# Kernel tuning notes

Measured on AMD Instinct MI355X. Metric: run time of the kernel, lower is better.

Reference implementation:

```python
import jax, jax.numpy as jnp
import numpy as np

N, E, G = 200000, 600000, 1024
NF_IN, EF_IN, H = 32, 16, 512
BN_EPS = 1e-5


def _bn(x, gamma, beta):
    # eval-mode BatchNorm1d with running_mean=0, running_var=1
    return x * (gamma / jnp.sqrt(1.0 + BN_EPS)) + beta


def setup_inputs() -> dict:
    key = jax.random.key(0)
    ks = jax.random.split(key, 32)
    s = 0.05
    inp = {
        'nf': jax.random.normal(ks[0], (N, NF_IN), jnp.float32),
        'ef': jax.random.normal(ks[1], (E, EF_IN), jnp.float32),
        'gf': jax.random.normal(ks[2], (G, H), jnp.float32),
        'device_params': jax.random.uniform(ks[3], (N,), jnp.float32),
        'node_y': jax.random.randint(ks[4], (N,), 0, 9),
        'batch_idx': jnp.sort(jax.random.randint(ks[5], (N,), 0, G)),
        'edge_index': jax.random.randint(ks[6], (2, E), 0, N),
        'nf_w1': jax.random.normal(ks[7], (NF_IN + 9, H), jnp.float32) * s,
        'nf_b1': jax.random.normal(ks[8], (H,), jnp.float32) * s,
        'nf_g1': jax.random.uniform(ks[9], (H,), jnp.float32, 0.5, 1.5),
        'nf_be1': jax.random.normal(ks[10], (H,), jnp.float32) * s,
        'nf_w2': jax.random.normal(ks[11], (H, H), jnp.float32) * s,
        'nf_b2': jax.random.normal(ks[12], (H,), jnp.float32) * s,
        'ef_w1': jax.random.normal(ks[13], (EF_IN, H), jnp.float32) * s,
        'ef_b1': jax.random.normal(ks[14], (H,), jnp.float32) * s,
        'ef_g1': jax.random.uniform(ks[15], (H,), jnp.float32, 0.5, 1.5),
        'ef_be1': jax.random.normal(ks[16], (H,), jnp.float32) * s,
        'ef_w2': jax.random.normal(ks[17], (H, H), jnp.float32) * s,
        'ef_b2': jax.random.normal(ks[18], (H,), jnp.float32) * s,
        'ow1': jax.random.normal(ks[19], (H, H), jnp.float32) * s,
        'ob1': jax.random.normal(ks[20], (H,), jnp.float32) * s,
        'og1': jax.random.uniform(ks[21], (H,), jnp.float32, 0.5, 1.5),
        'obe1': jax.random.normal(ks[22], (H,), jnp.float32) * s,
        'ow2': jax.random.normal(ks[23], (H, H), jnp.float32) * s,
        'ob2': jax.random.normal(ks[24], (H,), jnp.float32) * s,
        'og2': jax.random.uniform(ks[25], (H,), jnp.float32, 0.5, 1.5),
        'obe2': jax.random.normal(ks[26], (H,), jnp.float32) * s,
        'ow3': jax.random.normal(ks[27], (H, 2), jnp.float32) * s,
        'ob3': jax.random.normal(ks[28], (2,), jnp.float32) * s,
    }
    return inp


def reference(nf, ef, gf, device_params, node_y, batch_idx, edge_index,
              nf_w1, nf_b1, nf_g1, nf_be1, nf_w2, nf_b2,
              ef_w1, ef_b1, ef_g1, ef_be1, ef_w2, ef_b2,
              ow1, ob1, og1, obe1, ow2, ob2, og2, obe2, ow3, ob3):
    num_graphs = gf.shape[0]
    gelu = lambda x: jax.nn.gelu(x, approximate=False)  # torch nn.GELU default

    # DeviceParam_MLP: augment node features with scaled one-hot of node class
    nf_aug = jnp.concatenate(
        [nf, jax.nn.one_hot(node_y, 9, dtype=nf.dtype) * device_params[:, None]],
        axis=-1)  # [N, nf_in+9]
    h_n = gelu(_bn(nf_aug @ nf_w1 + nf_b1, nf_g1, nf_be1)) @ nf_w2 + nf_b2  # [N,H]
    h_e = gelu(_bn(ef @ ef_w1 + ef_b1, ef_g1, ef_be1)) @ ef_w2 + ef_b2      # [E,H]

    # two scatter_add pools into graph features
    gh = gf
    gh = gh + jax.ops.segment_sum(h_n, batch_idx, num_segments=num_graphs)
    edge_graph = batch_idx[edge_index[0]]  # graph id of each edge's source node
    gh = gh + jax.ops.segment_sum(h_e, edge_graph, num_segments=num_graphs)

    # output MLP (layer_num=3): two hidden blocks + final Linear -> 2
    x = gelu(_bn(gh @ ow1 + ob1, og1, obe1))
    x = gelu(_bn(x @ ow2 + ob2, og2, obe2))
    return x @ ow3 + ob3  # [G, 2]
```

## Files before the change

kernel.cpp:

```cpp
#include <hip/hip_runtime.h>
#include <hip/hip_bf16.h>

#define NN 200000
#define NE 600000
#define NG 1024
#define HH 512
#define ECAP 1024

typedef short short8 __attribute__((ext_vector_type(8)));
typedef float f32x4 __attribute__((ext_vector_type(4)));
typedef float f32x2 __attribute__((ext_vector_type(2)));

__device__ __forceinline__ unsigned short f2bf(float f){
  unsigned u = __float_as_uint(f);
  u += 0x7fffu + ((u >> 16) & 1u);
  return (unsigned short)(u >> 16);
}
__device__ __forceinline__ float bf2f(unsigned short h){
  return __uint_as_float(((unsigned)h) << 16);
}

__device__ __forceinline__ short8 cvt8pk(float4 a, float4 b){
  union { short8 s; __hip_bfloat162 h[4]; } u;
  u.h[0] = __float22bfloat162_rn(make_float2(a.x, a.y));
  u.h[1] = __float22bfloat162_rn(make_float2(a.z, a.w));
  u.h[2] = __float22bfloat162_rn(make_float2(b.x, b.y));
  u.h[3] = __float22bfloat162_rn(make_float2(b.z, b.w));
  return u.s;
}

__device__ __forceinline__ void split8(const float* v, short8* hi, short8* lo){
  union { short8 s; __hip_bfloat162 h[4]; unsigned u[4]; } H, L;
#pragma unroll
  for (int p=0;p<4;++p){
    float a = v[2*p], b = v[2*p+1];
    H.h[p] = __float22bfloat162_rn(make_float2(a, b));
    unsigned hu = H.u[p];
    L.h[p] = __float22bfloat162_rn(make_float2(a - __uint_as_float(hu << 16),
                                               b - __uint_as_float(hu & 0xffff0000u)));
  }
  *hi = H.s; *lo = L.s;
}

__device__ __forceinline__ float gelu_f(float x){
  float p = __builtin_fmaf(x*x, -0.10294325f, -2.3022085f);
  float e = __builtin_amdgcn_exp2f(x * p);
  return x * __builtin_amdgcn_rcpf(1.0f + e);
}

__device__ __forceinline__ float gelu_poly(float x,
    float C0, float C1, float C2, float C3, float C4, float C5, float C6, float C7){
  float u = x*x;
  float s = __builtin_fmaf(u, 0.125f, -1.0f);
  float p = C7;
  p = __builtin_fmaf(p, s, C6); p = __builtin_fmaf(p, s, C5);
  p = __builtin_fmaf(p, s, C4); p = __builtin_fmaf(p, s, C3);
  p = __builtin_fmaf(p, s, C2); p = __builtin_fmaf(p, s, C1);
  p = __builtin_fmaf(p, s, C0);
  return __builtin_fmaf(x, 0.5f, p);
}

__device__ __forceinline__ void gelu2_acc(f32x2 x, f32x2& dst,
    float C0, float C1, float C2, float C3, float C4, float C5, float C6, float C7){
  f32x2 u = x*x;
  f32x2 s = __builtin_elementwise_fma(u, (f32x2)0.125f, (f32x2)(-1.0f));
  f32x2 p = (f32x2)C7;
  p = __builtin_elementwise_fma(p, s, (f32x2)C6);
  p = __builtin_elementwise_fma(p, s, (f32x2)C5);
  p = __builtin_elementwise_fma(p, s, (f32x2)C4);
  p = __builtin_elementwise_fma(p, s, (f32x2)C3);
  p = __builtin_elementwise_fma(p, s, (f32x2)C2);
  p = __builtin_elementwise_fma(p, s, (f32x2)C1);
  p = __builtin_elementwise_fma(p, s, (f32x2)C0);
  dst += __builtin_elementwise_fma(x, (f32x2)0.5f, p);
}

__global__ __launch_bounds__(256) void kpre(
    const float* __restrict__ nfw1, const float* __restrict__ nfb1,
    const float* __restrict__ nfg1, const float* __restrict__ nfbe1,
    const float* __restrict__ efw1, const float* __restrict__ efb1,
    const float* __restrict__ efg1, const float* __restrict__ efbe1,
    unsigned short* __restrict__ w1nT, unsigned short* __restrict__ w1eT,
    float* __restrict__ b1n, float* __restrict__ b1e,
    const int* __restrict__ bidx, int* __restrict__ nstart,
    int* __restrict__ cnt, float* __restrict__ pcoef,
    const float* __restrict__ nf, const float* __restrict__ dp,
    const int* __restrict__ ny,
    unsigned short* __restrict__ nfb, unsigned short* __restrict__ hb){
  const float rs = 0.99999500003750f;
  int b = blockIdx.x, t = threadIdx.x;
  if (b < 196){
    int tid = b*256 + t;
    if (tid < 512*64){
      int c = tid >> 6, k = tid & 63;
      float w = (k < 41) ? nfw1[k*HH + c] * nfg1[c] * rs : 0.0f;
      w1nT[tid] = f2bf(w);
    } else if (tid < 512*96){
      int u = tid - 512*64; int c = u >> 5, k = u & 31;
      float w = (k < 16) ? efw1[k*HH + c] * efg1[c] * rs : 0.0f;
      w1eT[u] = f2bf(w);
    } else if (tid < 512*96 + 512){
      int c = tid - 512*96;
      b1n[c] = nfb1[c]*nfg1[c]*rs + nfbe1[c];
    } else if (tid < 512*96 + 1024){
      int c = tid - (512*96 + 512);
      b1e[c] = efb1[c]*efg1[c]*rs + efbe1[c];
    }
  } else if (b < 978){
    int i = (b-196)*256 + t;
    if (i < NN){
      int g0 = bidx[i];
      int g1 = (i+1 < NN) ? bidx[i+1] : NG;
      for (int g = g0+1; g <= g1; ++g) nstart[g] = i+1;
      if (i == 0) for (int g = 0; g <= g0; ++g) nstart[g] = 0;
    }
  } else if (b == 978){
    cnt[t] = 0; cnt[t+256] = 0; cnt[t+512] = 0; cnt[t+768] = 0;
  } else if (b == 979){
    if (t == 0){
      double th[8], fj[8];
      for (int j=0;j<8;++j){
        th[j] = 3.14159265358979323846*((double)j + 0.5)/8.0;
        double cs = cos(th[j]);
        double u = 8.0*(cs + 1.0);
        double v = sqrt(u);
        fj[j] = 0.5*v*erf(v*0.70710678118654752);
      }
      double c[8];
      for (int k=0;k<8;++k){
        double sm = 0.0;
        for (int j=0;j<8;++j) sm += fj[j]*cos((double)k*th[j]);
        c[k] = 0.25*sm;
      }
      c[0] *= 0.5;
      const double T[8][8] = {
        { 1, 0,  0,  0,   0,    0,  0,  0},
        { 0, 1,  0,  0,   0,    0,  0,  0},
        {-1, 0,  2,  0,   0,    0,  0,  0},
        { 0,-3,  0,  4,   0,    0,  0,  0},
        { 1, 0, -8,  0,   8,    0,  0,  0},
        { 0, 5,  0,-20,   0,   16,  0,  0},
        {-1, 0, 18,  0, -48,    0, 32,  0},
        { 0,-7,  0, 56,   0, -112,  0, 64}};
      double m[8] = {0,0,0,0,0,0,0,0};
      for (int k=0;k<8;++k)
        for (int i=0;i<8;++i) m[i] += c[k]*T[k][i];
      double p0 = m[0]-m[1]+m[2]-m[3]+m[4]-m[5]+m[6]-m[7];
      m[0] -= p0;
      for (int i=0;i<8;++i) pcoef[i] = (float)m[i];
    }
  } else {
    int r = (b-980)*256 + t;
    if (r < NN){
      const float4* ap = (const float4*)(nf + (size_t)r*32);
      unsigned short* op = nfb + (size_t)r*32;
#pragma unroll
      for (int p2=0; p2<4; ++p2){
        short8 s = cvt8pk(ap[2*p2], ap[2*p2+1]);
        *(short8*)(op + 8*p2) = s;
      }
      unsigned short db = f2bf(dp[r]);
      int cls = ny[r];
      short8 h0, h1;
#pragma unroll
      for (int j=0;j<8;++j) h0[j] = (cls==j) ? (short)db : (short)0;
      h1 = (short8){0,0,0,0,0,0,0,0};
      h1[0] = (cls==8) ? (short)db : (short)0;
      unsigned short* hp = hb + (size_t)r*16;
      *(short8*)hp = h0;
      *(short8*)(hp + 8) = h1;
    }
  }
}

__global__ __launch_bounds__(1024) void kscatter(const int* __restrict__ eidx,
    const int* __restrict__ bidx, int* __restrict__ eg,
    int* __restrict__ cnt, int* __restrict__ perm2d){
  __shared__ int h[NG];
  __shared__ int base[NG];
  const int b = blockIdx.x, t = threadIdx.x;
  h[t] = 0;
  __syncthreads();
  const int per = NE / 64;
  const int lo = b*per, hi = lo + per;
  for (int e = lo + t; e < hi; e += 1024){
    int g = bidx[eidx[e]];
    eg[e] = g;
    atomicAdd(&h[g], 1);
  }
  __syncthreads();
  int c = h[t];
  if (c > 0) base[t] = atomicAdd(&cnt[t], c);
  h[t] = 0;
  __syncthreads();
  for (int e = lo + t; e < hi; e += 1024){
    int g = eg[e];
    int p = base[g] + atomicAdd(&h[g], 1);
    perm2d[(g << 10) + p] = e;
  }
}

__global__ __launch_bounds__(256) void kmain(
    const unsigned short* __restrict__ nfb, const unsigned short* __restrict__ hb,
    const int* __restrict__ nstart, const float* __restrict__ ef,
    const int* __restrict__ perm2d, const int* __restrict__ cnt,
    const unsigned short* __restrict__ w1nT, const unsigned short* __restrict__ w1eT,
    const float* __restrict__ b1n, const float* __restrict__ b1e,
    const float* __restrict__ pcoef, float* __restrict__ S){
  const int t = threadIdx.x;
  const int lane = t & 63, w = t >> 6;
  const int q = lane >> 4, m = lane & 15;
  const float C0 = pcoef[0], C1 = pcoef[1], C2 = pcoef[2], C3 = pcoef[3];
  const float C4 = pcoef[4], C5 = pcoef[5], C6 = pcoef[6], C7 = pcoef[7];
  const short8 zz = {0,0,0,0,0,0,0,0};
  if (blockIdx.x < 2048){
    const int g = blockIdx.x >> 1;
    const int c0 = ((blockIdx.x & 1) << 8) + (w << 6);
    short8 bfr[4]; float bias[4];
    f32x2 cacc[4] = {{0.f,0.f},{0.f,0.f},{0.f,0.f},{0.f,0.f}};
#pragma unroll
    for (int nt=0; nt<4; ++nt){
      int c = c0 + (nt<<4) + m;
      bfr[nt] = *(const short8*)(w1eT + (c << 5) + (q << 3));
      bias[nt] = b1e[c];
    }
    const int base = g << 10;
    const int s1 = cnt[g];
    const int nfull = s1 >> 4;
    int rb = 0;
    for (int ch=0; ch<nfull; ++ch, rb += 16){
      int e = perm2d[base + rb + m];
      short8 f = zz;
      if (q < 2){
        const float4* ap = (const float4*)(ef + (size_t)e*16 + (q<<3));
        f = cvt8pk(ap[0], ap[1]);
      }
#pragma unroll
      for (int nt=0; nt<4; ++nt){
        f32x4 acc = {bias[nt], bias[nt], bias[nt], bias[nt]};
        acc = __builtin_amdgcn_mfma_f32_16x16x32_bf16(f, bfr[nt], acc, 0, 0, 0);
        f32x2 xlo = {acc[0], acc[1]}, xhi = {acc[2], acc[3]};
        gelu2_acc(xlo, cacc[nt], C0,C1,C2,C3,C4,C5,C6,C7);
        gelu2_acc(xhi, cacc[nt], C0,C1,C2,C3,C4,C5,C6,C7);
      }
    }
    if (rb < s1){
      int row = rb + m;
      int e = perm2d[base + ((row < s1) ? row : 0)];
      short8 f = zz;
      if (q < 2){
        const float4* ap = (const float4*)(ef + (size_t)e*16 + (q<<3));
        f = cvt8pk(ap[0], ap[1]);
      }
      const int vr = s1 - rb;
#pragma unroll
      for (int nt=0; nt<4; ++nt){
        f32x4 acc = {bias[nt], bias[nt], bias[nt], bias[nt]};
        acc = __builtin_amdgcn_mfma_f32_16x16x32_bf16(f, bfr[nt], acc, 0, 0, 0);
#pragma unroll
        for (int i=0;i<4;++i){
          float gv = (((q<<2)+i) < vr) ? gelu_poly(acc[i], C0,C1,C2,C3,C4,C5,C6,C7) : 0.f;
          cacc[nt].x += gv;
        }
      }
    }
#pragma unroll
    for (int nt=0; nt<4; ++nt){
      float s = cacc[nt].x + cacc[nt].y;
      s += __shfl_xor(s, 16); s += __shfl_xor(s, 32);
      if (lane < 16) S[(size_t)g*1024 + 512 + c0 + (nt<<4) + lane] = s;
    }
  } else {
    const int b2 = blockIdx.x - 2048;
    const int g = b2 >> 2;
    const int c0 = ((b2 & 3) << 7) + (w << 5);
    short8 bf0[2], bf1[2]; float bias[2];
    f32x2 cacc[2] = {{0.f,0.f},{0.f,0.f}};
#pragma unroll
    for (int nt=0; nt<2; ++nt){
      int c = c0 + (nt<<4) + m;
      const short8* bp = (const short8*)(w1nT + (c << 6) + (q << 3));
      bf0[nt] = bp[0]; bf1[nt] = bp[4];
      bias[nt] = b1n[c];
    }
    const int s0 = nstart[g], s1 = nstart[g+1];
    const int nfull = (s1 - s0) >> 4;
    int rb = s0;
    for (int ch=0; ch<nfull; ++ch, rb += 16){
      int ar = rb + m;
      short8 f = *(const short8*)(nfb + (size_t)ar*32 + (q<<3));
      short8 h = (q < 2) ? *(const short8*)(hb + (size_t)ar*16 + (q<<3)) : zz;
#pragma unroll
      for (int nt=0; nt<2; ++nt){
        f32x4 acc = {bias[nt], bias[nt], bias[nt], bias[nt]};
        acc = __builtin_amdgcn_mfma_f32_16x16x32_bf16(f, bf0[nt], acc, 0, 0, 0);
        acc = __builtin_amdgcn_mfma_f32_16x16x32_bf16(h, bf1[nt], acc, 0, 0, 0);
        f32x2 xlo = {acc[0], acc[1]}, xhi = {acc[2], acc[3]};
        gelu2_acc(xlo, cacc[nt], C0,C1,C2,C3,C4,C5,C6,C7);
        gelu2_acc(xhi, cacc[nt], C0,C1,C2,C3,C4,C5,C6,C7);
      }
    }
    if (rb < s1){
      int row = rb + m;
      int ar = (row < s1) ? row : s0;
      short8 f = *(const short8*)(nfb + (size_t)ar*32 + (q<<3));
      short8 h = (q < 2) ? *(const short8*)(hb + (size_t)ar*16 + (q<<3)) : zz;
      const int vr = s1 - rb;
#pragma unroll
      for (int nt=0; nt<2; ++nt){
        f32x4 acc = {bias[nt], bias[nt], bias[nt], bias[nt]};
        acc = __builtin_amdgcn_mfma_f32_16x16x32_bf16(f, bf0[nt], acc, 0, 0, 0);
        acc = __builtin_amdgcn_mfma_f32_16x16x32_bf16(h, bf1[nt], acc, 0, 0, 0);
#pragma unroll
        for (int i=0;i<4;++i){
          float gv = (((q<<2)+i) < vr) ? gelu_poly(acc[i], C0,C1,C2,C3,C4,C5,C6,C7) : 0.f;
          cacc[nt].x += gv;
        }
      }
    }
#pragma unroll
    for (int nt=0; nt<2; ++nt){
      float s = cacc[nt].x + cacc[nt].y;
      s += __shfl_xor(s, 16); s += __shfl_xor(s, 32);
      if (lane < 16) S[(size_t)g*1024 + c0 + (nt<<4) + lane] = s;
    }
  }
}

__global__ __launch_bounds__(256) void kgemm3(const float* __restrict__ A, int lda, int nkc,
    const float* __restrict__ B0, const float* __restrict__ B1,
    float* __restrict__ out,
    const float* __restrict__ gf, const int* __restrict__ nstart, const int* __restrict__ cnt,
    const float* __restrict__ b2n, const float* __restrict__ b2e,
    const float* __restrict__ bias, const float* __restrict__ gam, const float* __restrict__ bet){
  const int t = threadIdx.x, lane = t & 63, w = t >> 6;
  const int q = lane >> 4, m = lane & 15;
  const int c0 = blockIdx.x*32, r0 = blockIdx.y*64 + w*16;
  f32x4 acc[2] = {{0.f,0.f,0.f,0.f},{0.f,0.f,0.f,0.f}};
  const float* ap = A + (size_t)(r0 + m)*lda + (q<<3);
  for (int kc = 0; kc < nkc; ++kc){
    const int ko = kc*32;
    float4 x = *(const float4*)(ap + ko);
    float4 y = *(const float4*)(ap + ko + 4);
    float v[8] = {x.x,x.y,x.z,x.w,y.x,y.y,y.z,y.w};
    short8 ah, al;
    split8(v, &ah, &al);
    const float* Bp = (kc < 16) ? B0 : B1;
    const float* bp = Bp + (size_t)((kc & 15)*32 + (q<<3))*HH + c0 + m;
#pragma unroll
    for (int cf=0; cf<2; ++cf){
      float bv[8];
#pragma unroll
      for (int j=0;j<8;++j) bv[j] = bp[(size_t)j*HH + cf*16];
      short8 bh, bl;
      split8(bv, &bh, &bl);
      acc[cf] = __builtin_amdgcn_mfma_f32_16x16x32_bf16(ah, bh, acc[cf], 0, 0, 0);
      acc[cf] = __builtin_amdgcn_mfma_f32_16x16x32_bf16(ah, bl, acc[cf], 0, 0, 0);
      acc[cf] = __builtin_amdgcn_mfma_f32_16x16x32_bf16(al, bh, acc[cf], 0, 0, 0);
    }
  }
  const float rs = 0.99999500003750f;
#pragma unroll
  for (int cf=0; cf<2; ++cf){
    int c = c0 + cf*16 + m;
    if (gf){
      const float bnv = b2n[c], bev = b2e[c];
#pragma unroll
      for (int i=0;i<4;++i){
        int r = blockIdx.y*64 + w*16 + q*4 + i;
        float cn = (float)(nstart[r+1] - nstart[r]);
        float ce = (float)cnt[r];
        float vv = acc[cf][i] + gf[(size_t)r*HH + c] + cn*bnv + ce*bev;
        out[(size_t)r*HH + c] = vv;
      }
    } else {
      const float sc = gam[c]*rs, bi = bias[c], be = bet[c];
#pragma unroll
      for (int i=0;i<4;++i){
        int r = blockIdx.y*64 + w*16 + q*4 + i;
        float vv = gelu_f((acc[cf][i] + bi)*sc + be);
        out[(size_t)r*HH + c] = vv;
      }
    }
  }
}

__global__ __launch_bounds__(256) void kfinal(const float* __restrict__ x2, const float* __restrict__ w3,
    const float* __restrict__ b3, float* __restrict__ out){
  const int lane = threadIdx.x & 63, wv = threadIdx.x >> 6;
  const int r = blockIdx.x*4 + wv;
  float a0 = 0.f, a1 = 0.f;
#pragma unroll
  for (int tt=0; tt<8; ++tt){
    int k = lane + tt*64;
    float x = x2[(size_t)r*HH + k];
    a0 = __builtin_fmaf(x, w3[2*k], a0);
    a1 = __builtin_fmaf(x, w3[2*k+1], a1);
  }
#pragma unroll
  for (int d=1; d<64; d<<=1){ a0 += __shfl_xor(a0, d); a1 += __shfl_xor(a1, d); }
  if (lane == 0){ out[r*2] = a0 + b3[0]; out[r*2+1] = a1 + b3[1]; }
}

extern "C" void kernel_launch(void* const* d_in, const int* in_sizes, int n_in,
                              void* d_out, int out_size, void* d_ws, size_t ws_size,
                              hipStream_t stream) {
  const float* nf    = (const float*)d_in[0];
  const float* ef    = (const float*)d_in[1];
  const float* gf    = (const float*)d_in[2];
  const float* dp    = (const float*)d_in[3];
  const int*   ny    = (const int*)d_in[4];
  const int*   bidx  = (const int*)d_in[5];
  const int*   eidx  = (const int*)d_in[6];
  const float* nfw1  = (const float*)d_in[7];
  const float* nfb1  = (const float*)d_in[8];
  const float* nfg1  = (const float*)d_in[9];
  const float* nfbe1 = (const float*)d_in[10];
  const float* w2n   = (const float*)d_in[11];
  const float* b2n   = (const float*)d_in[12];
  const float* efw1  = (const float*)d_in[13];
  const float* efb1  = (const float*)d_in[14];
  const float* efg1  = (const float*)d_in[15];
  const float* efbe1 = (const float*)d_in[16];
  const float* w2e   = (const float*)d_in[17];
  const float* b2e   = (const float*)d_in[18];
  const float* ow1   = (const float*)d_in[19];
  const float* ob1   = (const float*)d_in[20];
  const float* og1   = (const float*)d_in[21];
  const float* obe1  = (const float*)d_in[22];
  const float* ow2   = (const float*)d_in[23];
  const float* ob2   = (const float*)d_in[24];
  const float* og2   = (const float*)d_in[25];
  const float* obe2  = (const float*)d_in[26];
  const float* ow3   = (const float*)d_in[27];
  const float* ob3   = (const float*)d_in[28];

  unsigned char* p = (unsigned char*)d_ws;
  float* S      = (float*)p;                 p += (size_t)NG*1024*4;
  int*   perm2d = (int*)p;                   p += (size_t)NG*ECAP*4;
  int*   eg     = (int*)p;                   p += (size_t)NE*4;
  unsigned short* nfb = (unsigned short*)p;  p += (size_t)NN*32*2;
  unsigned short* hb  = (unsigned short*)p;  p += (size_t)NN*16*2;
  unsigned short* w1nT = (unsigned short*)p; p += 512*64*2;
  unsigned short* w1eT = (unsigned short*)p; p += 512*32*2;
  float* b1n    = (float*)p;                 p += 512*4;
  float* b1e    = (float*)p;                 p += 512*4;
  int* nstart   = (int*)p;                   p += 1032*4;
  int* cnt      = (int*)p;                   p += NG*4;
  float* pcoef  = (float*)p;                 p += 64;
  float* gh  = (float*)nfb;
  float* xg2 = gh  + (size_t)NG*HH;
  float* x2f = xg2 + (size_t)NG*HH;

  kpre<<<1762, 256, 0, stream>>>(nfw1, nfb1, nfg1, nfbe1, efw1, efb1, efg1, efbe1,
                                 w1nT, w1eT, b1n, b1e, bidx, nstart, cnt, pcoef,
                                 nf, dp, ny, nfb, hb);
  kscatter<<<64, 1024, 0, stream>>>(eidx, bidx, eg, cnt, perm2d);
  kmain<<<6144, 256, 0, stream>>>(nfb, hb, nstart, ef, perm2d, cnt,
                                  w1nT, w1eT, b1n, b1e, pcoef, S);
  kgemm3<<<dim3(16,16), 256, 0, stream>>>(S, 1024, 32, w2n, w2e, gh,
                                          gf, nstart, cnt, b2n, b2e,
                                          nullptr, nullptr, nullptr);
  kgemm3<<<dim3(16,16), 256, 0, stream>>>(gh, 512, 16, ow1, ow1, xg2,
                                          nullptr, nullptr, nullptr, nullptr, nullptr,
                                          ob1, og1, obe1);
  kgemm3<<<dim3(16,16), 256, 0, stream>>>(xg2, 512, 16, ow2, ow2, x2f,
                                          nullptr, nullptr, nullptr, nullptr, nullptr,
                                          ob2, og2, obe2);
  kfinal<<<NG/4, 256, 0, stream>>>(x2f, ow3, ob3, (float*)d_out);
}
```

Baseline: 350.0 us.

## Split edge/node first-layer kernels onto 32x32 MFMA with bf16 pre-converted inputs

Replaces the combined kmain with separate kedge and knode kernels. Both use 32x32x16 bf16 MFMA tiles, and kedge double-buffers gathered edge rows through LDS. The preprocessing kernel now converts edge features to bf16 and packs node features plus the one-hot block into a 48-wide bf16 row. Weights and biases are prescaled by 1/sqrt(8) so the GELU polynomial saves one multiply, with the linear term factored out. The output GEMMs move to 16-column tiles with twice as many blocks, and perm2d writes gain an ECAP bound check. This adds an extra full pass over the edge features and more launches, in exchange for fewer, wider MFMAs and less per-edge conversion work.

```diff
diff --git a/kernel.cpp b/kernel.cpp
--- a/kernel.cpp
+++ b/kernel.cpp
@@ -10,6 +10,7 @@
 typedef short short8 __attribute__((ext_vector_type(8)));
 typedef float f32x4 __attribute__((ext_vector_type(4)));
 typedef float f32x2 __attribute__((ext_vector_type(2)));
+typedef float f32x16 __attribute__((ext_vector_type(16)));
 
 __device__ __forceinline__ unsigned short f2bf(float f){
   unsigned u = __float_as_uint(f);
@@ -48,75 +49,59 @@
   return x * __builtin_amdgcn_rcpf(1.0f + e);
 }
 
-__device__ __forceinline__ float gelu_poly(float x,
+__device__ __forceinline__ void g2(f32x2 xp, f32x2& aX, f32x2& aP,
     float C0, float C1, float C2, float C3, float C4, float C5, float C6, float C7){
-  float u = x*x;
-  float s = __builtin_fmaf(u, 0.125f, -1.0f);
-  float p = C7;
-  p = __builtin_fmaf(p, s, C6); p = __builtin_fmaf(p, s, C5);
-  p = __builtin_fmaf(p, s, C4); p = __builtin_fmaf(p, s, C3);
-  p = __builtin_fmaf(p, s, C2); p = __builtin_fmaf(p, s, C1);
-  p = __builtin_fmaf(p, s, C0);
-  return __builtin_fmaf(x, 0.5f, p);
-}
-
-__device__ __forceinline__ void gelu2_acc(f32x2 x, f32x2& dst,
-    float C0, float C1, float C2, float C3, float C4, float C5, float C6, float C7){
-  f32x2 u = x*x;
-  f32x2 s = __builtin_elementwise_fma(u, (f32x2)0.125f, (f32x2)(-1.0f));
-  f32x2 p = (f32x2)C7;
-  p = __builtin_elementwise_fma(p, s, (f32x2)C6);
+  f32x2 s = __builtin_elementwise_fma(xp, xp, (f32x2)(-1.0f));
+  f32x2 p = __builtin_elementwise_fma(s, (f32x2)C7, (f32x2)C6);
   p = __builtin_elementwise_fma(p, s, (f32x2)C5);
   p = __builtin_elementwise_fma(p, s, (f32x2)C4);
   p = __builtin_elementwise_fma(p, s, (f32x2)C3);
   p = __builtin_elementwise_fma(p, s, (f32x2)C2);
   p = __builtin_elementwise_fma(p, s, (f32x2)C1);
   p = __builtin_elementwise_fma(p, s, (f32x2)C0);
-  dst += __builtin_elementwise_fma(x, (f32x2)0.5f, p);
-}
+  aX += xp; aP += p;
+}
+
+#define ISQ 0.35355339059327376f
+#define SQ2 1.41421356237309505f
 
 __global__ __launch_bounds__(256) void kpre(
     const float* __restrict__ nfw1, const float* __restrict__ nfb1,
     const float* __restrict__ nfg1, const float* __restrict__ nfbe1,
     const float* __restrict__ efw1, const float* __restrict__ efb1,
     const float* __restrict__ efg1, const float* __restrict__ efbe1,
-    unsigned short* __restrict__ w1nT, unsigned short* __restrict__ w1eT,
-    float* __restrict__ b1n, float* __restrict__ b1e,
+    unsigned short* __restrict__ w1n48T, unsigned short* __restrict__ w1eT16,
+    float* __restrict__ b1n_s, float* __restrict__ b1e_s,
     const int* __restrict__ bidx, int* __restrict__ nstart,
     int* __restrict__ cnt, float* __restrict__ pcoef,
     const float* __restrict__ nf, const float* __restrict__ dp,
-    const int* __restrict__ ny,
-    unsigned short* __restrict__ nfb, unsigned short* __restrict__ hb){
+    const int* __restrict__ ny, const float* __restrict__ ef,
+    unsigned short* __restrict__ nf48, unsigned short* __restrict__ efb){
   const float rs = 0.99999500003750f;
   int b = blockIdx.x, t = threadIdx.x;
-  if (b < 196){
-    int tid = b*256 + t;
-    if (tid < 512*64){
-      int c = tid >> 6, k = tid & 63;
-      float w = (k < 41) ? nfw1[k*HH + c] * nfg1[c] * rs : 0.0f;
-      w1nT[tid] = f2bf(w);
-    } else if (tid < 512*96){
-      int u = tid - 512*64; int c = u >> 5, k = u & 31;
-      float w = (k < 16) ? efw1[k*HH + c] * efg1[c] * rs : 0.0f;
-      w1eT[u] = f2bf(w);
-    } else if (tid < 512*96 + 512){
-      int c = tid - 512*96;
-      b1n[c] = nfb1[c]*nfg1[c]*rs + nfbe1[c];
-    } else if (tid < 512*96 + 1024){
-      int c = tid - (512*96 + 512);
-      b1e[c] = efb1[c]*efg1[c]*rs + efbe1[c];
-    }
-  } else if (b < 978){
-    int i = (b-196)*256 + t;
+  if (b < 2){
+    int c = b*256 + t;
+    float sc = efg1[c]*rs*ISQ;
+#pragma unroll
+    for (int k=0;k<16;++k) w1eT16[c*16+k] = f2bf(efw1[k*HH+c]*sc);
+    b1e_s[c] = (efb1[c]*efg1[c]*rs + efbe1[c])*ISQ;
+  } else if (b < 4){
+    int c = (b-2)*256 + t;
+    float sc = nfg1[c]*rs*ISQ;
+#pragma unroll
+    for (int k=0;k<48;++k)
+      w1n48T[c*48+k] = (k < 41) ? f2bf(nfw1[k*HH+c]*sc) : (unsigned short)0;
+    b1n_s[c] = (nfb1[c]*nfg1[c]*rs + nfbe1[c])*ISQ;
+  } else if (b < 786){
+    int i = (b-4)*256 + t;
     if (i < NN){
       int g0 = bidx[i];
       int g1 = (i+1 < NN) ? bidx[i+1] : NG;
       for (int g = g0+1; g <= g1; ++g) nstart[g] = i+1;
       if (i == 0) for (int g = 0; g <= g0; ++g) nstart[g] = 0;
     }
-  } else if (b == 978){
+  } else if (b == 786){
     cnt[t] = 0; cnt[t+256] = 0; cnt[t+512] = 0; cnt[t+768] = 0;
-  } else if (b == 979){
     if (t == 0){
       double th[8], fj[8];
       for (int j=0;j<8;++j){
@@ -149,26 +134,35 @@
       m[0] -= p0;
       for (int i=0;i<8;++i) pcoef[i] = (float)m[i];
     }
-  } else {
-    int r = (b-980)*256 + t;
+  } else if (b < 1569){
+    int r = (b-787)*256 + t;
     if (r < NN){
       const float4* ap = (const float4*)(nf + (size_t)r*32);
-      unsigned short* op = nfb + (size_t)r*32;
+      unsigned short v[48];
+      union { short8 s; unsigned short u[8]; } cv;
 #pragma unroll
       for (int p2=0; p2<4; ++p2){
-        short8 s = cvt8pk(ap[2*p2], ap[2*p2+1]);
-        *(short8*)(op + 8*p2) = s;
+        cv.s = cvt8pk(ap[2*p2], ap[2*p2+1]);
+#pragma unroll
+        for (int j=0;j<8;++j) v[p2*8+j] = cv.u[j];
       }
       unsigned short db = f2bf(dp[r]);
       int cls = ny[r];
-      short8 h0, h1;
-#pragma unroll
-      for (int j=0;j<8;++j) h0[j] = (cls==j) ? (short)db : (short)0;
-      h1 = (short8){0,0,0,0,0,0,0,0};
-      h1[0] = (cls==8) ? (short)db : (short)0;
-      unsigned short* hp = hb + (size_t)r*16;
-      *(short8*)hp = h0;
-      *(short8*)(hp + 8) = h1;
+#pragma unroll
+      for (int j=0;j<9;++j) v[32+j] = (cls==j) ? db : (unsigned short)0;
+#pragma unroll
+      for (int j=41;j<48;++j) v[j] = 0;
+      unsigned short* op = nf48 + (size_t)r*48;
+#pragma unroll
+      for (int p2=0; p2<6; ++p2) *(short8*)(op + p2*8) = *(short8*)&v[p2*8];
+    }
+  } else {
+    int r = (b-1569)*256 + t;
+    if (r < NE){
+      const float4* ap = (const float4*)(ef + (size_t)r*16);
+      unsigned short* op = efb + (size_t)r*16;
+      *(short8*)op       = cvt8pk(ap[0], ap[1]);
+      *(short8*)(op + 8) = cvt8pk(ap[2], ap[3]);
     }
   }
 }
@@ -196,135 +190,129 @@
   for (int e = lo + t; e < hi; e += 1024){
     int g = eg[e];
     int p = base[g] + atomicAdd(&h[g], 1);
-    perm2d[(g << 10) + p] = e;
-  }
-}
-
-__global__ __launch_bounds__(256) void kmain(
-    const unsigned short* __restrict__ nfb, const unsigned short* __restrict__ hb,
-    const int* __restrict__ nstart, const float* __restrict__ ef,
-    const int* __restrict__ perm2d, const int* __restrict__ cnt,
-    const unsigned short* __restrict__ w1nT, const unsigned short* __restrict__ w1eT,
-    const float* __restrict__ b1n, const float* __restrict__ b1e,
+    if (p < ECAP) perm2d[(g << 10) + p] = e;
+  }
+}
+
+__global__ __launch_bounds__(512) void kedge(
+    const unsigned short* __restrict__ efb, const int* __restrict__ perm2d,
+    const int* __restrict__ cnt, const unsigned short* __restrict__ w1eT16,
+    const float* __restrict__ b1e_s, const float* __restrict__ pcoef,
+    float* __restrict__ S){
+  __shared__ short lds[2][32*40];
+  const int t = threadIdx.x;
+  const int lane = t & 63, wid = t >> 6;
+  const int hi = lane >> 5;
+  const int g = blockIdx.x >> 1;
+  const int col = ((blockIdx.x & 1) << 8) + (wid << 5) + (lane & 31);
+  const float C0 = pcoef[0], C1 = pcoef[1], C2 = pcoef[2], C3 = pcoef[3];
+  const float C4 = pcoef[4], C5 = pcoef[5], C6 = pcoef[6], C7 = pcoef[7];
+  short8 bfr = *(const short8*)(w1eT16 + col*16 + (hi<<3));
+  float bv = b1e_s[col];
+  f32x16 bias16;
+#pragma unroll
+  for (int i=0;i<16;++i) bias16[i] = bv;
+  f32x2 aX = {0.f,0.f}, aP = {0.f,0.f};
+  const int s1 = cnt[g];
+  if (s1 > 0){
+    const int base = g << 10;
+    const int nch = (s1 + 31) >> 5;
+    short8 a1;
+    if (t < 64){
+      int r0 = min(t & 31, s1-1);
+      int r1 = min(32 + (t & 31), s1-1);
+      int e0 = perm2d[base + r0];
+      int e1 = perm2d[base + r1];
+      short8 a0 = *(const short8*)(efb + (size_t)e0*16 + ((t>>5)<<3));
+      *(short8*)&lds[0][(t&31)*40 + ((t>>5)<<3)] = a0;
+      a1 = *(const short8*)(efb + (size_t)e1*16 + ((t>>5)<<3));
+    }
+    __syncthreads();
+    for (int ch=0; ch<nch; ++ch){
+      short8 af = *(const short8*)&lds[ch&1][(lane&31)*40 + (hi<<3)];
+      if (t < 64){
+        if (ch+1 < nch) *(short8*)&lds[(ch+1)&1][(t&31)*40 + ((t>>5)<<3)] = a1;
+        int r2 = min((ch+2)*32 + (t & 31), s1-1);
+        int e2 = perm2d[base + r2];
+        a1 = *(const short8*)(efb + (size_t)e2*16 + ((t>>5)<<3));
+      }
+      __syncthreads();
+      f32x16 acc = __builtin_amdgcn_mfma_f32_32x32x16_bf16(af, bfr, bias16, 0, 0, 0);
+      const int vr = s1 - ch*32;
+      if (vr >= 32){
+#pragma unroll
+        for (int i=0;i<8;++i){
+          f32x2 xp = {acc[2*i], acc[2*i+1]};
+          g2(xp, aX, aP, C0,C1,C2,C3,C4,C5,C6,C7);
+        }
+      } else {
+#pragma unroll
+        for (int i=0;i<8;++i){
+          int r0 = ((2*i)&3) + (((2*i)>>2)<<3) + (hi<<2);
+          f32x2 xp = { (r0 < vr) ? acc[2*i] : 0.f,
+                       (r0+1 < vr) ? acc[2*i+1] : 0.f };
+          g2(xp, aX, aP, C0,C1,C2,C3,C4,C5,C6,C7);
+        }
+      }
+    }
+  }
+  float ssum = __builtin_fmaf(SQ2, aX[0]+aX[1], aP[0]+aP[1]);
+  ssum += __shfl_xor(ssum, 32);
+  if (lane < 32) S[(size_t)g*1024 + 512 + col] = ssum;
+}
+
+__global__ __launch_bounds__(256) void knode(
+    const unsigned short* __restrict__ nf48, const int* __restrict__ nstart,
+    const unsigned short* __restrict__ w1n48T, const float* __restrict__ b1n_s,
     const float* __restrict__ pcoef, float* __restrict__ S){
   const int t = threadIdx.x;
-  const int lane = t & 63, w = t >> 6;
-  const int q = lane >> 4, m = lane & 15;
+  const int lane = t & 63, wid = t >> 6;
+  const int hi = lane >> 5;
+  const int g = blockIdx.x >> 2;
+  const int col = ((blockIdx.x & 3) << 7) + (wid << 5) + (lane & 31);
   const float C0 = pcoef[0], C1 = pcoef[1], C2 = pcoef[2], C3 = pcoef[3];
   const float C4 = pcoef[4], C5 = pcoef[5], C6 = pcoef[6], C7 = pcoef[7];
-  const short8 zz = {0,0,0,0,0,0,0,0};
-  if (blockIdx.x < 2048){
-    const int g = blockIdx.x >> 1;
-    const int c0 = ((blockIdx.x & 1) << 8) + (w << 6);
-    short8 bfr[4]; float bias[4];
-    f32x2 cacc[4] = {{0.f,0.f},{0.f,0.f},{0.f,0.f},{0.f,0.f}};
-#pragma unroll
-    for (int nt=0; nt<4; ++nt){
-      int c = c0 + (nt<<4) + m;
-      bfr[nt] = *(const short8*)(w1eT + (c << 5) + (q << 3));
-      bias[nt] = b1e[c];
-    }
-    const int base = g << 10;
-    const int s1 = cnt[g];
-    const int nfull = s1 >> 4;
-    int rb = 0;
-    for (int ch=0; ch<nfull; ++ch, rb += 16){
-      int e = perm2d[base + rb + m];
-      short8 f = zz;
-      if (q < 2){
-        const float4* ap = (const float4*)(ef + (size_t)e*16 + (q<<3));
-        f = cvt8pk(ap[0], ap[1]);
-      }
-#pragma unroll
-      for (int nt=0; nt<4; ++nt){
-        f32x4 acc = {bias[nt], bias[nt], bias[nt], bias[nt]};
-        acc = __builtin_amdgcn_mfma_f32_16x16x32_bf16(f, bfr[nt], acc, 0, 0, 0);
-        f32x2 xlo = {acc[0], acc[1]}, xhi = {acc[2], acc[3]};
-        gelu2_acc(xlo, cacc[nt], C0,C1,C2,C3,C4,C5,C6,C7);
-        gelu2_acc(xhi, cacc[nt], C0,C1,C2,C3,C4,C5,C6,C7);
-      }
-    }
-    if (rb < s1){
-      int row = rb + m;
-      int e = perm2d[base + ((row < s1) ? row : 0)];
-      short8 f = zz;
-      if (q < 2){
-        const float4* ap = (const float4*)(ef + (size_t)e*16 + (q<<3));
-        f = cvt8pk(ap[0], ap[1]);
-      }
-      const int vr = s1 - rb;
-#pragma unroll
-      for (int nt=0; nt<4; ++nt){
-        f32x4 acc = {bias[nt], bias[nt], bias[nt], bias[nt]};
-        acc = __builtin_amdgcn_mfma_f32_16x16x32_bf16(f, bfr[nt], acc, 0, 0, 0);
-#pragma unroll
-        for (int i=0;i<4;++i){
-          float gv = (((q<<2)+i) < vr) ? gelu_poly(acc[i], C0,C1,C2,C3,C4,C5,C6,C7) : 0.f;
-          cacc[nt].x += gv;
-        }
-      }
-    }
-#pragma unroll
-    for (int nt=0; nt<4; ++nt){
-      float s = cacc[nt].x + cacc[nt].y;
-      s += __shfl_xor(s, 16); s += __shfl_xor(s, 32);
-      if (lane < 16) S[(size_t)g*1024 + 512 + c0 + (nt<<4) + lane] = s;
-    }
-  } else {
-    const int b2 = blockIdx.x - 2048;
-    const int g = b2 >> 2;
-    const int c0 = ((b2 & 3) << 7) + (w << 5);
-    short8 bf0[2], bf1[2]; float bias[2];
-    f32x2 cacc[2] = {{0.f,0.f},{0.f,0.f}};
-#pragma unroll
-    for (int nt=0; nt<2; ++nt){
-      int c = c0 + (nt<<4) + m;
-      const short8* bp = (const short8*)(w1nT + (c << 6) + (q << 3));
-      bf0[nt] = bp[0]; bf1[nt] = bp[4];
-      bias[nt] = b1n[c];
-    }
-    const int s0 = nstart[g], s1 = nstart[g+1];
-    const int nfull = (s1 - s0) >> 4;
-    int rb = s0;
-    for (int ch=0; ch<nfull; ++ch, rb += 16){
-      int ar = rb + m;
-      short8 f = *(const short8*)(nfb + (size_t)ar*32 + (q<<3));
-      short8 h = (q < 2) ? *(const short8*)(hb + (size_t)ar*16 + (q<<3)) : zz;
-#pragma unroll
-      for (int nt=0; nt<2; ++nt){
-        f32x4 acc = {bias[nt], bias[nt], bias[nt], bias[nt]};
-        acc = __builtin_amdgcn_mfma_f32_16x16x32_bf16(f, bf0[nt], acc, 0, 0, 0);
-        acc = __builtin_amdgcn_mfma_f32_16x16x32_bf16(h, bf1[nt], acc, 0, 0, 0);
-        f32x2 xlo = {acc[0], acc[1]}, xhi = {acc[2], acc[3]};
-        gelu2_acc(xlo, cacc[nt], C0,C1,C2,C3,C4,C5,C6,C7);
-        gelu2_acc(xhi, cacc[nt], C0,C1,C2,C3,C4,C5,C6,C7);
-      }
-    }
-    if (rb < s1){
-      int row = rb + m;
-      int ar = (row < s1) ? row : s0;
-      short8 f = *(const short8*)(nfb + (size_t)ar*32 + (q<<3));
-      short8 h = (q < 2) ? *(const short8*)(hb + (size_t)ar*16 + (q<<3)) : zz;
-      const int vr = s1 - rb;
-#pragma unroll
-      for (int nt=0; nt<2; ++nt){
-        f32x4 acc = {bias[nt], bias[nt], bias[nt], bias[nt]};
-        acc = __builtin_amdgcn_mfma_f32_16x16x32_bf16(f, bf0[nt], acc, 0, 0, 0);
-        acc = __builtin_amdgcn_mfma_f32_16x16x32_bf16(h, bf1[nt], acc, 0, 0, 0);
-#pragma unroll
-        for (int i=0;i<4;++i){
-          float gv = (((q<<2)+i) < vr) ? gelu_poly(acc[i], C0,C1,C2,C3,C4,C5,C6,C7) : 0.f;
-          cacc[nt].x += gv;
-        }
-      }
-    }
-#pragma unroll
-    for (int nt=0; nt<2; ++nt){
-      float s = cacc[nt].x + cacc[nt].y;
-      s += __shfl_xor(s, 16); s += __shfl_xor(s, 32);
-      if (lane < 16) S[(size_t)g*1024 + c0 + (nt<<4) + lane] = s;
-    }
-  }
+  const unsigned short* bp = w1n48T + col*48 + (hi<<3);
+  short8 bf0 = *(const short8*)(bp);
+  short8 bf1 = *(const short8*)(bp + 16);
+  short8 bf2 = *(const short8*)(bp + 32);
+  float bv = b1n_s[col];
+  f32x16 bias16;
+#pragma unroll
+  for (int i=0;i<16;++i) bias16[i] = bv;
+  f32x2 aX = {0.f,0.f}, aP = {0.f,0.f};
+  const int s0 = nstart[g], s1 = nstart[g+1];
+  const int nch = (s1 - s0 + 31) >> 5;
+  for (int ch=0; ch<nch; ++ch){
+    int rb = s0 + ch*32;
+    int ar = min(rb + (lane & 31), s1-1);
+    const unsigned short* apn = nf48 + (size_t)ar*48 + (hi<<3);
+    short8 a0 = *(const short8*)(apn);
+    short8 a1 = *(const short8*)(apn + 16);
+    short8 a2 = *(const short8*)(apn + 32);
+    f32x16 acc = __builtin_amdgcn_mfma_f32_32x32x16_bf16(a0, bf0, bias16, 0, 0, 0);
+    acc = __builtin_amdgcn_mfma_f32_32x32x16_bf16(a1, bf1, acc, 0, 0, 0);
+    acc = __builtin_amdgcn_mfma_f32_32x32x16_bf16(a2, bf2, acc, 0, 0, 0);
+    const int vr = s1 - rb;
+    if (vr >= 32){
+#pragma unroll
+      for (int i=0;i<8;++i){
+        f32x2 xp = {acc[2*i], acc[2*i+1]};
+        g2(xp, aX, aP, C0,C1,C2,C3,C4,C5,C6,C7);
+      }
+    } else {
+#pragma unroll
+      for (int i=0;i<8;++i){
+        int r0 = ((2*i)&3) + (((2*i)>>2)<<3) + (hi<<2);
+        f32x2 xp = { (r0 < vr) ? acc[2*i] : 0.f,
+                     (r0+1 < vr) ? acc[2*i+1] : 0.f };
+        g2(xp, aX, aP, C0,C1,C2,C3,C4,C5,C6,C7);
+      }
+    }
+  }
+  float ssum = __builtin_fmaf(SQ2, aX[0]+aX[1], aP[0]+aP[1]);
+  ssum += __shfl_xor(ssum, 32);
+  if (lane < 32) S[(size_t)g*1024 + col] = ssum;
 }
 
 __global__ __launch_bounds__(256) void kgemm3(const float* __restrict__ A, int lda, int nkc,
@@ -335,8 +323,8 @@
     const float* __restrict__ bias, const float* __restrict__ gam, const float* __restrict__ bet){
   const int t = threadIdx.x, lane = t & 63, w = t >> 6;
   const int q = lane >> 4, m = lane & 15;
-  const int c0 = blockIdx.x*32, r0 = blockIdx.y*64 + w*16;
-  f32x4 acc[2] = {{0.f,0.f,0.f,0.f},{0.f,0.f,0.f,0.f}};
+  const int c0 = blockIdx.x*16, r0 = blockIdx.y*64 + w*16;
+  f32x4 acc = {0.f,0.f,0.f,0.f};
   const float* ap = A + (size_t)(r0 + m)*lda + (q<<3);
   for (int kc = 0; kc < nkc; ++kc){
     const int ko = kc*32;
@@ -347,40 +335,32 @@
     split8(v, &ah, &al);
     const float* Bp = (kc < 16) ? B0 : B1;
     const float* bp = Bp + (size_t)((kc & 15)*32 + (q<<3))*HH + c0 + m;
-#pragma unroll
-    for (int cf=0; cf<2; ++cf){
-      float bv[8];
-#pragma unroll
-      for (int j=0;j<8;++j) bv[j] = bp[(size_t)j*HH + cf*16];
-      short8 bh, bl;
-      split8(bv, &bh, &bl);
-      acc[cf] = __builtin_amdgcn_mfma_f32_16x16x32_bf16(ah, bh, acc[cf], 0, 0, 0);
-      acc[cf] = __builtin_amdgcn_mfma_f32_16x16x32_bf16(ah, bl, acc[cf], 0, 0, 0);
-      acc[cf] = __builtin_amdgcn_mfma_f32_16x16x32_bf16(al, bh, acc[cf], 0, 0, 0);
-    }
+    float bvv[8];
+#pragma unroll
+    for (int j=0;j<8;++j) bvv[j] = bp[(size_t)j*HH];
+    short8 bh, bl;
+    split8(bvv, &bh, &bl);
+    acc = __builtin_amdgcn_mfma_f32_16x16x32_bf16(ah, bh, acc, 0, 0, 0);
+    acc = __builtin_amdgcn_mfma_f32_16x16x32_bf16(ah, bl, acc, 0, 0, 0);
+    acc = __builtin_amdgcn_mfma_f32_16x16x32_bf16(al, bh, acc, 0, 0, 0);
   }
   const float rs = 0.99999500003750f;
-#pragma unroll
-  for (int cf=0; cf<2; ++cf){
-    int c = c0 + cf*16 + m;
-    if (gf){
-      const float bnv = b2n[c], bev = b2e[c];
-#pragma unroll
-      for (int i=0;i<4;++i){
-        int r = blockIdx.y*64 + w*16 + q*4 + i;
-        float cn = (float)(nstart[r+1] - nstart[r]);
-        float ce = (float)cnt[r];
-        float vv = acc[cf][i] + gf[(size_t)r*HH + c] + cn*bnv + ce*bev;
-        out[(size_t)r*HH + c] = vv;
-      }
-    } else {
-      const float sc = gam[c]*rs, bi = bias[c], be = bet[c];
-#pragma unroll
-      for (int i=0;i<4;++i){
-        int r = blockIdx.y*64 + w*16 + q*4 + i;
-        float vv = gelu_f((acc[cf][i] + bi)*sc + be);
-        out[(size_t)r*HH + c] = vv;
-      }
+  const int c = c0 + m;
+  if (gf){
+    const float bnv = b2n[c], bev = b2e[c];
+#pragma unroll
+    for (int i=0;i<4;++i){
+      int r = r0 + q*4 + i;
+      float cn = (float)(nstart[r+1] - nstart[r]);
+      float ce = (float)cnt[r];
+      out[(size_t)r*HH + c] = acc[i] + gf[(size_t)r*HH + c] + cn*bnv + ce*bev;
+    }
+  } else {
+    const float sc = gam[c]*rs, bi = bias[c], be = bet[c];
+#pragma unroll
+    for (int i=0;i<4;++i){
+      int r = r0 + q*4 + i;
+      out[(size_t)r*HH + c] = gelu_f((acc[i] + bi)*sc + be);
     }
   }
 }
@@ -438,33 +418,33 @@
   unsigned char* p = (unsigned char*)d_ws;
   float* S      = (float*)p;                 p += (size_t)NG*1024*4;
   int*   perm2d = (int*)p;                   p += (size_t)NG*ECAP*4;
-  int*   eg     = (int*)p;                   p += (size_t)NE*4;
-  unsigned short* nfb = (unsigned short*)p;  p += (size_t)NN*32*2;
-  unsigned short* hb  = (unsigned short*)p;  p += (size_t)NN*16*2;
-  unsigned short* w1nT = (unsigned short*)p; p += 512*64*2;
-  unsigned short* w1eT = (unsigned short*)p; p += 512*32*2;
-  float* b1n    = (float*)p;                 p += 512*4;
-  float* b1e    = (float*)p;                 p += 512*4;
+  unsigned short* nf48 = (unsigned short*)p; p += (size_t)NN*48*2;
+  unsigned short* efb  = (unsigned short*)p; p += (size_t)NE*16*2;
+  unsigned short* w1n48T = (unsigned short*)p; p += 512*48*2;
+  unsigned short* w1eT16 = (unsigned short*)p; p += 512*16*2;
+  float* b1n_s  = (float*)p;                 p += 512*4;
+  float* b1e_s  = (float*)p;                 p += 512*4;
   int* nstart   = (int*)p;                   p += 1032*4;
   int* cnt      = (int*)p;                   p += NG*4;
   float* pcoef  = (float*)p;                 p += 64;
-  float* gh  = (float*)nfb;
+  int* eg = (int*)S;
+  float* gh  = (float*)nf48;
   float* xg2 = gh  + (size_t)NG*HH;
   float* x2f = xg2 + (size_t)NG*HH;
 
-  kpre<<<1762, 256, 0, stream>>>(nfw1, nfb1, nfg1, nfbe1, efw1, efb1, efg1, efbe1,
-                                 w1nT, w1eT, b1n, b1e, bidx, nstart, cnt, pcoef,
-                                 nf, dp, ny, nfb, hb);
+  kpre<<<3913, 256, 0, stream>>>(nfw1, nfb1, nfg1, nfbe1, efw1, efb1, efg1, efbe1,
+                                 w1n48T, w1eT16, b1n_s, b1e_s, bidx, nstart, cnt,
+                                 pcoef, nf, dp, ny, ef, nf48, efb);
   kscatter<<<64, 1024, 0, stream>>>(eidx, bidx, eg, cnt, perm2d);
-  kmain<<<6144, 256, 0, stream>>>(nfb, hb, nstart, ef, perm2d, cnt,
-                                  w1nT, w1eT, b1n, b1e, pcoef, S);
-  kgemm3<<<dim3(16,16), 256, 0, stream>>>(S, 1024, 32, w2n, w2e, gh,
+  kedge<<<2048, 512, 0, stream>>>(efb, perm2d, cnt, w1eT16, b1e_s, pcoef, S);
+  knode<<<4096, 256, 0, stream>>>(nf48, nstart, w1n48T, b1n_s, pcoef, S);
+  kgemm3<<<dim3(32,16), 256, 0, stream>>>(S, 1024, 32, w2n, w2e, gh,
                                           gf, nstart, cnt, b2n, b2e,
                                           nullptr, nullptr, nullptr);
-  kgemm3<<<dim3(16,16), 256, 0, stream>>>(gh, 512, 16, ow1, ow1, xg2,
+  kgemm3<<<dim3(32,16), 256, 0, stream>>>(gh, 512, 16, ow1, ow1, xg2,
                                           nullptr, nullptr, nullptr, nullptr, nullptr,
                                           ob1, og1, obe1);
-  kgemm3<<<dim3(16,16), 256, 0, stream>>>(xg2, 512, 16, ow2, ow2, x2f,
+  kgemm3<<<dim3(32,16), 256, 0, stream>>>(xg2, 512, 16, ow2, ow2, x2f,
                                           nullptr, nullptr, nullptr, nullptr, nullptr,
                                           ob2, og2, obe2);
   kfinal<<<NG/4, 256, 0, stream>>>(x2f, ow3, ob3, (float*)d_out);
```

After: 341.1 us. -2.6%, faster.
